# Performance work log

Measured on AMD Instinct MI355X. Metric: run time of the kernel, lower is better.

The kernel has to match this reference:

```python
import jax, jax.numpy as jnp
import numpy as np

TARGET_FRAMES = 16
VOXEL_LAMBDA = 20.0
CONF_THRESHOLD = 0.1
CONF_PERCENTILE = 50.0
G = 48  # per-axis voxel grid cap (lambda=20 => ~20-40 occupied cells/axis for randn points)


def setup_inputs() -> dict:
    key = jax.random.key(0)
    k1, k2, k3, k4, k5 = jax.random.split(key, 5)
    B, S, H, W = 1, 128, 224, 224
    return {
        "depth": jax.random.uniform(k1, (B, S, H, W, 1), dtype=jnp.float32),
        "depth_conf": jax.random.uniform(k2, (B, S, H, W), dtype=jnp.float32),
        "world_points": jax.random.normal(k3, (B, S, H, W, 3), dtype=jnp.float32),
        "world_points_conf": jax.random.uniform(k4, (B, S, H, W), dtype=jnp.float32),
        "pose_enc": jax.random.normal(k5, (B, S, 9), dtype=jnp.float32),
    }


def _voxel_occupancy(world_points, world_points_conf):
    # world_points: [1,S,H,W,3], conf: [1,S,H,W]
    pts = world_points[0].reshape(world_points.shape[1], -1, 3)   # [S, HW, 3]
    conf = world_points_conf[0].reshape(world_points.shape[1], -1)  # [S, HW]
    # per-frame confidence filter: conf > thr AND conf >= per-frame percentile
    pct = jnp.quantile(conf, CONF_PERCENTILE / 100.0, axis=1)       # [S]
    valid = (conf > CONF_THRESHOLD) & (conf >= pct[:, None])        # [S, HW]
    big = jnp.float32(1e30)
    pmin = jnp.min(jnp.where(valid[..., None], pts, big), axis=(0, 1))   # [3]
    pmax = jnp.max(jnp.where(valid[..., None], pts, -big), axis=(0, 1))  # [3]
    voxel_size = jnp.min(pmax - pmin) / VOXEL_LAMBDA  # adaptive voxel size
    idx = jnp.floor((pts - pmin) / voxel_size).astype(jnp.int32)
    idx = jnp.clip(idx, 0, G - 1)
    vid = (idx[..., 0] * G + idx[..., 1]) * G + idx[..., 2]  # [S, HW]
    V = G * G * G
    vid = jnp.where(valid, vid, V)  # invalid points -> trash bin V
    S = pts.shape[0]
    occ = jnp.zeros((S, V + 1), dtype=bool).at[jnp.arange(S)[:, None], vid].set(True)
    return occ[:, :V]  # [S, V] per-frame voxel occupancy bitmaps


def _greedy_max_coverage(occ, k):
    S, V = occ.shape

    def step(carry, _):
        covered, selected = carry  # [V] bool, [S] bool
        gains = jnp.sum(occ & ~covered[None, :], axis=1).astype(jnp.float32)  # [S]
        gains = jnp.where(selected, -1.0, gains)
        best = jnp.argmax(gains)  # first max == greedy in-order tie-break
        covered = covered | occ[best]
        selected = selected.at[best].set(True)
        return (covered, selected), (best.astype(jnp.int32), gains[best])

    (covered, _), (sel, scores) = jax.lax.scan(
        step, (jnp.zeros((V,), bool), jnp.zeros((S,), bool)), None, length=k)
    return sel, scores, covered


def reference(depth, depth_conf, world_points, world_points_conf, pose_enc):
    occ = _voxel_occupancy(world_points, world_points_conf)
    sel, scores, covered = _greedy_max_coverage(occ, TARGET_FRAMES)
    total_coverage = jnp.sum(covered).astype(jnp.int32)
    # selected_indices [1,K], coverage_scores [1,K], total_coverage scalar
    return sel[None, :], scores[None, :], total_coverage
```

## Files before the change

### kernel.cpp

```cpp
#include <hip/hip_runtime.h>
#include <cstdint>

#define S_FRAMES 128
#define HW       50176
#define NGRP     12544
#define HALFG    6272
#define NBINS    4096
#define CAP      512
#define KSEL     16
#define VBW      1568

#define PLW      1024u
#define RQ       13

#define PL_OFF   0u
#define MM_OFF   (256u*PLW)
#define UWI_OFF  (MM_OFF + 1024u)
#define PCT_OFF  (UWI_OFF + 16u)
#define VB_OFF   (PCT_OFF + 128u)
#define ZWORDS   (MM_OFF + 1024u + 16u)

__device__ __forceinline__ unsigned fkey(float f) {
    unsigned u = __float_as_uint(f);
    return (u & 0x80000000u) ? ~u : (u | 0x80000000u);
}
__device__ __forceinline__ float funkey(unsigned k) {
    unsigned u = (k & 0x80000000u) ? (k & 0x7fffffffu) : ~k;
    return __uint_as_float(u);
}

__global__ __launch_bounds__(1024) void pct_kernel(const float* __restrict__ conf,
                                                   float* __restrict__ pct,
                                                   unsigned* __restrict__ ws) {
    const int s = blockIdx.x;
    const int tid = threadIdx.x;
    const int lane = tid & 63, wid = tid >> 6;
    const float4* c4 = (const float4*)(conf + (size_t)s * HW);

    for (unsigned i = tid; i < 2057u; i += 1024u) {
        unsigned idx = (unsigned)s * 2057u + i;
        if (idx < ZWORDS) ws[idx] = 0u;
    }

    __shared__ unsigned hist[NBINS];
    __shared__ unsigned wtot[16];
    __shared__ unsigned woff[16];
    __shared__ float    list[CAP];
    __shared__ unsigned cnt;
    __shared__ int      rbin[2];
    __shared__ unsigned rcum[2];
    __shared__ float    ab[2];

    for (int b = tid; b < NBINS; b += 1024) hist[b] = 0;
    if (tid == 0) cnt = 0;
    __syncthreads();

    for (int g = tid; g < NGRP; g += 1024) {
        float4 v = c4[g];
        int b0 = min(max((int)(v.x * 4096.0f), 0), NBINS - 1);
        int b1 = min(max((int)(v.y * 4096.0f), 0), NBINS - 1);
        int b2 = min(max((int)(v.z * 4096.0f), 0), NBINS - 1);
        int b3 = min(max((int)(v.w * 4096.0f), 0), NBINS - 1);
        atomicAdd(&hist[b0], 1u); atomicAdd(&hist[b1], 1u);
        atomicAdd(&hist[b2], 1u); atomicAdd(&hist[b3], 1u);
    }
    __syncthreads();

    unsigned chunk = hist[tid * 4] + hist[tid * 4 + 1] + hist[tid * 4 + 2] + hist[tid * 4 + 3];
    unsigned x = chunk;
#pragma unroll
    for (int m = 1; m < 64; m <<= 1) {
        unsigned y = (unsigned)__shfl_up((int)x, m);
        if (lane >= m) x += y;
    }
    if (lane == 63) wtot[wid] = x;
    __syncthreads();
    if (tid < 16) {
        unsigned acc = 0;
        for (int w = 0; w < tid; w++) acc += wtot[w];
        woff[tid] = acc;
    }
    __syncthreads();
    unsigned excl = x - chunk + woff[wid];

    const unsigned R0 = 25087u, R1 = 25088u;
#pragma unroll
    for (int r = 0; r < 2; r++) {
        unsigned rr = r ? R1 : R0;
        if (rr >= excl && rr < excl + chunk) {
            unsigned cum = excl;
            for (int j = 0; j < 4; j++) {
                unsigned h = hist[tid * 4 + j];
                if (rr < cum + h) { rbin[r] = tid * 4 + j; rcum[r] = cum; break; }
                cum += h;
            }
        }
    }
    __syncthreads();

    const int blo = rbin[0], bhi = rbin[1];
    const unsigned cumLo = rcum[0];

    for (int g = tid; g < NGRP; g += 1024) {
        float4 v = c4[g];
        float vv[4] = {v.x, v.y, v.z, v.w};
#pragma unroll
        for (int j = 0; j < 4; j++) {
            int b = min(max((int)(vv[j] * 4096.0f), 0), NBINS - 1);
            if (b >= blo && b <= bhi) {
                unsigned pos = atomicAdd(&cnt, 1u);
                if (pos < CAP) list[pos] = vv[j];
            }
        }
    }
    __syncthreads();

    const int n = (int)min(cnt, (unsigned)CAP);
    const int r0 = (int)(R0 - cumLo), r1 = (int)(R1 - cumLo);
    for (int e = tid; e < n; e += 1024) {
        float xx = list[e];
        int rank = 0;
        for (int j = 0; j < n; j++) {
            float y = list[j];
            rank += (y < xx) || (y == xx && j < e);
        }
        if (rank == r0) ab[0] = xx;
        if (rank == r1) ab[1] = xx;
    }
    __syncthreads();
    if (tid == 0) pct[s] = 0.5f * ab[0] + 0.5f * ab[1];
}

__global__ __launch_bounds__(256) void minmax_kernel(const float* __restrict__ wp,
                                                     const float* __restrict__ conf,
                                                     const float* __restrict__ pct,
                                                     unsigned* __restrict__ ws) {
    const int s = blockIdx.y;
    const int tid = threadIdx.x;
    const int gidx = blockIdx.x * 256 + tid;
    const float pc = pct[s];
    const size_t base = (size_t)s * HW;

    const float4 cf = ((const float4*)(conf + base))[gidx];
    const float4* wp4 = (const float4*)(wp + base * 3) + (size_t)gidx * 3;
    const float4 a = wp4[0], b = wp4[1], d = wp4[2];

    const float BIG = 3.402823466e38f;
    float mnx = BIG, mny = BIG, mnz = BIG;
    float mxx = -BIG, mxy = -BIG, mxz = -BIG;

    float px[4] = {a.x, a.w, b.z, d.y};
    float py[4] = {a.y, b.x, b.w, d.z};
    float pz[4] = {a.z, b.y, d.x, d.w};
    float cc[4] = {cf.x, cf.y, cf.z, cf.w};
    unsigned nib = 0;
#pragma unroll
    for (int j = 0; j < 4; j++) {
        bool v = (cc[j] > 0.1f) && (cc[j] >= pc);
        nib |= (v ? 1u : 0u) << j;
        float x = v ? px[j] : BIG, y = v ? py[j] : BIG, z = v ? pz[j] : BIG;
        mnx = fminf(mnx, x); mny = fminf(mny, y); mnz = fminf(mnz, z);
        x = v ? px[j] : -BIG; y = v ? py[j] : -BIG; z = v ? pz[j] : -BIG;
        mxx = fmaxf(mxx, x); mxy = fmaxf(mxy, y); mxz = fmaxf(mxz, z);
    }

    __shared__ unsigned vbw[32];
    if (tid < 32) vbw[tid] = 0;
    __syncthreads();
    if (nib) atomicOr(&vbw[tid >> 3], nib << ((tid & 7) * 4));

#pragma unroll
    for (int m = 32; m >= 1; m >>= 1) {
        mnx = fminf(mnx, __shfl_xor(mnx, m)); mny = fminf(mny, __shfl_xor(mny, m));
        mnz = fminf(mnz, __shfl_xor(mnz, m));
        mxx = fmaxf(mxx, __shfl_xor(mxx, m)); mxy = fmaxf(mxy, __shfl_xor(mxy, m));
        mxz = fmaxf(mxz, __shfl_xor(mxz, m));
    }
    __shared__ float red[4][6];
    if ((tid & 63) == 0) {
        int w = tid >> 6;
        red[w][0] = mnx; red[w][1] = mny; red[w][2] = mnz;
        red[w][3] = mxx; red[w][4] = mxy; red[w][5] = mxz;
    }
    __syncthreads();
    if (tid < 32)
        ws[VB_OFF + (unsigned)s * 1568u + (unsigned)blockIdx.x * 32u + tid] = vbw[tid];
    if (tid == 0) {
        float r0 = red[0][0], r1 = red[0][1], r2 = red[0][2];
        float r3 = red[0][3], r4 = red[0][4], r5 = red[0][5];
        for (int w = 1; w < 4; w++) {
            r0 = fminf(r0, red[w][0]); r1 = fminf(r1, red[w][1]); r2 = fminf(r2, red[w][2]);
            r3 = fmaxf(r3, red[w][3]); r4 = fmaxf(r4, red[w][4]); r5 = fmaxf(r5, red[w][5]);
        }
        unsigned* slot = ws + MM_OFF + (unsigned)((blockIdx.x + blockIdx.y * 49) & 63) * 16;
        atomicMax(slot + 0, fkey(-r0));
        atomicMax(slot + 1, fkey(-r1));
        atomicMax(slot + 2, fkey(-r2));
        atomicMax(slot + 3, fkey(r3));
        atomicMax(slot + 4, fkey(r4));
        atomicMax(slot + 5, fkey(r5));
    }
}

__global__ __launch_bounds__(1024) void voxel_kernel(const float* __restrict__ wp,
                                                     unsigned* __restrict__ ws) {
    const int s = blockIdx.x >> 1;
    const int part = blockIdx.x & 1;
    const int tid = threadIdx.x;

    __shared__ unsigned bm[PLW];
    __shared__ float prm[4];
    __shared__ int   dsh[3];
    bm[tid] = 0;

    if (tid < 64) {
        const unsigned* sl = ws + MM_OFF + (unsigned)tid * 16;
        unsigned k0 = sl[0], k1 = sl[1], k2 = sl[2], k3 = sl[3], k4 = sl[4], k5 = sl[5];
#pragma unroll
        for (int m = 32; m >= 1; m >>= 1) {
            k0 = max(k0, (unsigned)__shfl_xor((int)k0, m));
            k1 = max(k1, (unsigned)__shfl_xor((int)k1, m));
            k2 = max(k2, (unsigned)__shfl_xor((int)k2, m));
            k3 = max(k3, (unsigned)__shfl_xor((int)k3, m));
            k4 = max(k4, (unsigned)__shfl_xor((int)k4, m));
            k5 = max(k5, (unsigned)__shfl_xor((int)k5, m));
        }
        if (tid == 0) {
            float p0 = -funkey(k0), p1 = -funkey(k1), p2 = -funkey(k2);
            float e0 = funkey(k3) - p0, e1 = funkey(k4) - p1, e2 = funkey(k5) - p2;
            float vs = fminf(e0, fminf(e1, e2)) / 20.0f;
            int Dx = min(48, (int)floorf(e0 / vs) + 1);
            int Dy = min(48, (int)floorf(e1 / vs) + 1);
            int Dz = min(48, (int)floorf(e2 / vs) + 1);
            int D  = Dx * Dy * Dz;
            prm[0] = p0; prm[1] = p1; prm[2] = p2; prm[3] = vs;
            dsh[0] = Dy; dsh[1] = Dz;
            unsigned uw = (unsigned)((D + 31) >> 5);
            dsh[2] = (int)min(uw, PLW);
            if (blockIdx.x == 0) ws[UWI_OFF] = uw;
        }
    }
    __syncthreads();

    const float pmx = prm[0], pmy = prm[1], pmz = prm[2], vs = prm[3];
    const int Dy = dsh[0], Dz = dsh[1], UWs = dsh[2];
    const size_t base = (size_t)s * HW;
    const float4* w4 = (const float4*)(wp + base * 3);
    const unsigned* vb = ws + VB_OFF + (unsigned)s * 1568u;

#pragma unroll 1
    for (int k = 0; k < 7; k++) {
        int gl = k * 1024 + tid;
        if (gl >= HALFG) break;
        int g = part * HALFG + gl;
        const float4* wg = w4 + (size_t)g * 3;
        float4 a = wg[0], b = wg[1], d = wg[2];
        unsigned nib = (vb[g >> 3] >> ((g & 7) * 4)) & 0xFu;
        if (nib) {
            float px[4] = {a.x, a.w, b.z, d.y};
            float py[4] = {a.y, b.x, b.w, d.z};
            float pz[4] = {a.z, b.y, d.x, d.w};
#pragma unroll
            for (int j = 0; j < 4; j++) {
                if ((nib >> j) & 1u) {
                    int ix = min(max((int)floorf((px[j] - pmx) / vs), 0), 47);
                    int iy = min(max((int)floorf((py[j] - pmy) / vs), 0), 47);
                    int iz = min(max((int)floorf((pz[j] - pmz) / vs), 0), 47);
                    int vid = (ix * Dy + iy) * Dz + iz;
                    if ((unsigned)vid < PLW * 32u)
                        atomicOr(&bm[vid >> 5], 1u << (vid & 31));
                }
            }
        }
    }
    __syncthreads();

    unsigned* occ = ws + PL_OFF + (unsigned)blockIdx.x * PLW;
    for (int w = tid; w < UWs; w += 1024) occ[w] = bm[w];
}

__global__ __launch_bounds__(1024, 1) void greedy1_kernel(unsigned* __restrict__ ws,
                                                          float* __restrict__ out) {
    const int tid = threadIdx.x;
    const int f = tid >> 3, sl = tid & 7;
    unsigned UW = ws[UWI_OFF];
    if (UW > PLW) UW = PLW;

    __shared__ unsigned cov[PLW];
    __shared__ int gains[S_FRAMES];
    __shared__ unsigned bestsh;

    for (int w = tid; w < (int)PLW; w += 1024) cov[w] = 0u;
    bool selF = false;
    int best = -1;

    if (UW <= 8u * RQ * 4u) {
        uint4 occw[RQ];
        const uint4* myA = (const uint4*)(ws + PL_OFF + (unsigned)(f * 2 + 0) * PLW) + sl * RQ;
        const uint4* myB = (const uint4*)(ws + PL_OFF + (unsigned)(f * 2 + 1) * PLW) + sl * RQ;
#pragma unroll
        for (int j = 0; j < RQ; j++) {
            uint4 a4 = myA[j], b4 = myB[j];
            occw[j].x = a4.x | b4.x; occw[j].y = a4.y | b4.y;
            occw[j].z = a4.z | b4.z; occw[j].w = a4.w | b4.w;
        }
        __syncthreads();

        for (int it = 0; it < KSEL; it++) {
            if (best >= 0 && f == best) {
#pragma unroll
                for (int j = 0; j < RQ; j++) {
                    int w = (sl * RQ + j) * 4;
                    cov[w] |= occw[j].x; cov[w + 1] |= occw[j].y;
                    cov[w + 2] |= occw[j].z; cov[w + 3] |= occw[j].w;
                }
            }
            __syncthreads();
            int g = 0;
#pragma unroll
            for (int j = 0; j < RQ; j++) {
                int w = (sl * RQ + j) * 4;
                g += __popc(occw[j].x & ~cov[w]) + __popc(occw[j].y & ~cov[w + 1])
                   + __popc(occw[j].z & ~cov[w + 2]) + __popc(occw[j].w & ~cov[w + 3]);
            }
            g += __shfl_xor(g, 1); g += __shfl_xor(g, 2); g += __shfl_xor(g, 4);
            if (sl == 0) gains[f] = selF ? -1 : g;
            __syncthreads();
            if (tid < 64) {
                int g1 = gains[tid], g2 = gains[tid + 64];
                unsigned k1 = (g1 < 0) ? 0u : (((unsigned)g1 << 7) | (unsigned)(127 - tid));
                unsigned k2 = (g2 < 0) ? 0u : (((unsigned)g2 << 7) | (unsigned)(63 - tid));
                unsigned k = max(k1, k2);
#pragma unroll
                for (int m = 32; m >= 1; m >>= 1) k = max(k, (unsigned)__shfl_xor((int)k, m));
                if (tid == 0) {
                    bestsh = k;
                    out[it] = (float)(127 - (int)(k & 127u));
                    out[KSEL + it] = (float)(k >> 7);
                }
            }
            __syncthreads();
            best = 127 - (int)(bestsh & 127u);
            if (f == best) selF = true;
        }
        if (f == best) {
#pragma unroll
            for (int j = 0; j < RQ; j++) {
                int w = (sl * RQ + j) * 4;
                cov[w] |= occw[j].x; cov[w + 1] |= occw[j].y;
                cov[w + 2] |= occw[j].z; cov[w + 3] |= occw[j].w;
            }
        }
        __syncthreads();
        if (f == 0) {
            int t = 0;
#pragma unroll
            for (int j = 0; j < RQ; j++) {
                int w = (sl * RQ + j) * 4;
                t += __popc(cov[w]) + __popc(cov[w + 1]) + __popc(cov[w + 2]) + __popc(cov[w + 3]);
            }
            t += __shfl_xor(t, 1); t += __shfl_xor(t, 2); t += __shfl_xor(t, 4);
            if (sl == 0) out[2 * KSEL] = (float)t;
        }
    } else {
        const int Q = (int)((UW + 31) >> 5);
        const uint4* myA = (const uint4*)(ws + PL_OFF + (unsigned)(f * 2 + 0) * PLW) + sl * Q;
        const uint4* myB = (const uint4*)(ws + PL_OFF + (unsigned)(f * 2 + 1) * PLW) + sl * Q;
        __syncthreads();

        for (int it = 0; it < KSEL; it++) {
            if (best >= 0 && f == best) {
                const uint4* bA = (const uint4*)(ws + PL_OFF + (unsigned)(best * 2 + 0) * PLW) + sl * Q;
                const uint4* bB = (const uint4*)(ws + PL_OFF + (unsigned)(best * 2 + 1) * PLW) + sl * Q;
#pragma unroll 4
                for (int j = 0; j < Q; j++) {
                    uint4 oa = bA[j], ob = bB[j];
                    int w = (sl * Q + j) * 4;
                    cov[w] |= oa.x | ob.x; cov[w + 1] |= oa.y | ob.y;
                    cov[w + 2] |= oa.z | ob.z; cov[w + 3] |= oa.w | ob.w;
                }
            }
            __syncthreads();
            int g = 0;
#pragma unroll 4
            for (int j = 0; j < Q; j++) {
                uint4 oa = myA[j], ob = myB[j];
                int w = (sl * Q + j) * 4;
                g += __popc((oa.x | ob.x) & ~cov[w]) + __popc((oa.y | ob.y) & ~cov[w + 1])
                   + __popc((oa.z | ob.z) & ~cov[w + 2]) + __popc((oa.w | ob.w) & ~cov[w + 3]);
            }
            g += __shfl_xor(g, 1); g += __shfl_xor(g, 2); g += __shfl_xor(g, 4);
            if (sl == 0) gains[f] = selF ? -1 : g;
            __syncthreads();
            if (tid < 64) {
                int g1 = gains[tid], g2 = gains[tid + 64];
                unsigned k1 = (g1 < 0) ? 0u : (((unsigned)g1 << 7) | (unsigned)(127 - tid));
                unsigned k2 = (g2 < 0) ? 0u : (((unsigned)g2 << 7) | (unsigned)(63 - tid));
                unsigned k = max(k1, k2);
#pragma unroll
                for (int m = 32; m >= 1; m >>= 1) k = max(k, (unsigned)__shfl_xor((int)k, m));
                if (tid == 0) {
                    bestsh = k;
                    out[it] = (float)(127 - (int)(k & 127u));
                    out[KSEL + it] = (float)(k >> 7);
                }
            }
            __syncthreads();
            best = 127 - (int)(bestsh & 127u);
            if (f == best) selF = true;
        }
        if (f == best) {
            const uint4* bA = (const uint4*)(ws + PL_OFF + (unsigned)(best * 2 + 0) * PLW) + sl * Q;
            const uint4* bB = (const uint4*)(ws + PL_OFF + (unsigned)(best * 2 + 1) * PLW) + sl * Q;
#pragma unroll 4
            for (int j = 0; j < Q; j++) {
                uint4 oa = bA[j], ob = bB[j];
                int w = (sl * Q + j) * 4;
                cov[w] |= oa.x | ob.x; cov[w + 1] |= oa.y | ob.y;
                cov[w + 2] |= oa.z | ob.z; cov[w + 3] |= oa.w | ob.w;
            }
        }
        __syncthreads();
        if (f == 0) {
            int t = 0;
#pragma unroll 4
            for (int j = 0; j < Q; j++) {
                int w = (sl * Q + j) * 4;
                t += __popc(cov[w]) + __popc(cov[w + 1]) + __popc(cov[w + 2]) + __popc(cov[w + 3]);
            }
            t += __shfl_xor(t, 1); t += __shfl_xor(t, 2); t += __shfl_xor(t, 4);
            if (sl == 0) out[2 * KSEL] = (float)t;
        }
    }
}

extern "C" void kernel_launch(void* const* d_in, const int* in_sizes, int n_in,
                              void* d_out, int out_size, void* d_ws, size_t ws_size,
                              hipStream_t stream) {
    const float* wp   = (const float*)d_in[2];
    const float* conf = (const float*)d_in[3];
    float* out = (float*)d_out;
    unsigned* ws = (unsigned*)d_ws;
    float* pct = (float*)(ws + PCT_OFF);

    pct_kernel<<<128, 1024, 0, stream>>>(conf, pct, ws);
    minmax_kernel<<<dim3(49, 128), 256, 0, stream>>>(wp, conf, pct, ws);
    voxel_kernel<<<256, 1024, 0, stream>>>(wp, ws);
    greedy1_kernel<<<1, 1024, 0, stream>>>(ws, out);
}
```

Measured before the change: 227.6 us.

## Split per-frame confidence histogram into quarter-frame blocks before percentile select

```diff
diff --git a/kernel.cpp b/kernel.cpp
--- a/kernel.cpp
+++ b/kernel.cpp
@@ -4,6 +4,7 @@
 #define S_FRAMES 128
 #define HW       50176
 #define NGRP     12544
+#define QGRP     3136
 #define HALFG    6272
 #define NBINS    4096
 #define CAP      512
@@ -18,6 +19,7 @@
 #define UWI_OFF  (MM_OFF + 1024u)
 #define PCT_OFF  (UWI_OFF + 16u)
 #define VB_OFF   (PCT_OFF + 128u)
+#define H4_OFF   (VB_OFF + 128u*VBW)
 #define ZWORDS   (MM_OFF + 1024u + 16u)
 
 __device__ __forceinline__ unsigned fkey(float f) {
@@ -29,18 +31,45 @@
     return __uint_as_float(u);
 }
 
-__global__ __launch_bounds__(1024) void pct_kernel(const float* __restrict__ conf,
-                                                   float* __restrict__ pct,
-                                                   unsigned* __restrict__ ws) {
+__global__ __launch_bounds__(1024) void hist4_kernel(const float* __restrict__ conf,
+                                                     unsigned* __restrict__ ws) {
+    const int s = blockIdx.x >> 2;
+    const int q = blockIdx.x & 3;
+    const int tid = threadIdx.x;
+    const float4* c4 = (const float4*)(conf + (size_t)s * HW);
+
+    if (tid < 515) {
+        unsigned idx = (unsigned)blockIdx.x * 515u + tid;
+        if (idx < ZWORDS) ws[idx] = 0u;
+    }
+
+    __shared__ unsigned hist[NBINS];
+    for (int b = tid; b < NBINS; b += 1024) hist[b] = 0;
+    __syncthreads();
+
+    const int g0 = q * QGRP;
+    for (int gl = tid; gl < QGRP; gl += 1024) {
+        float4 v = c4[g0 + gl];
+        int b0 = min(max((int)(v.x * 4096.0f), 0), NBINS - 1);
+        int b1 = min(max((int)(v.y * 4096.0f), 0), NBINS - 1);
+        int b2 = min(max((int)(v.z * 4096.0f), 0), NBINS - 1);
+        int b3 = min(max((int)(v.w * 4096.0f), 0), NBINS - 1);
+        atomicAdd(&hist[b0], 1u); atomicAdd(&hist[b1], 1u);
+        atomicAdd(&hist[b2], 1u); atomicAdd(&hist[b3], 1u);
+    }
+    __syncthreads();
+
+    unsigned* out = ws + H4_OFF + (unsigned)blockIdx.x * NBINS;
+    for (int b = tid; b < NBINS; b += 1024) out[b] = hist[b];
+}
+
+__global__ __launch_bounds__(1024) void select_kernel(const float* __restrict__ conf,
+                                                      float* __restrict__ pct,
+                                                      unsigned* __restrict__ ws) {
     const int s = blockIdx.x;
     const int tid = threadIdx.x;
     const int lane = tid & 63, wid = tid >> 6;
     const float4* c4 = (const float4*)(conf + (size_t)s * HW);
-
-    for (unsigned i = tid; i < 2057u; i += 1024u) {
-        unsigned idx = (unsigned)s * 2057u + i;
-        if (idx < ZWORDS) ws[idx] = 0u;
-    }
 
     __shared__ unsigned hist[NBINS];
     __shared__ unsigned wtot[16];
@@ -51,19 +80,13 @@
     __shared__ unsigned rcum[2];
     __shared__ float    ab[2];
 
-    for (int b = tid; b < NBINS; b += 1024) hist[b] = 0;
+    const unsigned* q0 = ws + H4_OFF + (unsigned)(s * 4 + 0) * NBINS;
+    const unsigned* q1 = ws + H4_OFF + (unsigned)(s * 4 + 1) * NBINS;
+    const unsigned* q2 = ws + H4_OFF + (unsigned)(s * 4 + 2) * NBINS;
+    const unsigned* q3 = ws + H4_OFF + (unsigned)(s * 4 + 3) * NBINS;
+    for (int b = tid; b < NBINS; b += 1024)
+        hist[b] = q0[b] + q1[b] + q2[b] + q3[b];
     if (tid == 0) cnt = 0;
-    __syncthreads();
-
-    for (int g = tid; g < NGRP; g += 1024) {
-        float4 v = c4[g];
-        int b0 = min(max((int)(v.x * 4096.0f), 0), NBINS - 1);
-        int b1 = min(max((int)(v.y * 4096.0f), 0), NBINS - 1);
-        int b2 = min(max((int)(v.z * 4096.0f), 0), NBINS - 1);
-        int b3 = min(max((int)(v.w * 4096.0f), 0), NBINS - 1);
-        atomicAdd(&hist[b0], 1u); atomicAdd(&hist[b1], 1u);
-        atomicAdd(&hist[b2], 1u); atomicAdd(&hist[b3], 1u);
-    }
     __syncthreads();
 
     unsigned chunk = hist[tid * 4] + hist[tid * 4 + 1] + hist[tid * 4 + 2] + hist[tid * 4 + 3];
@@ -443,7 +466,8 @@
     unsigned* ws = (unsigned*)d_ws;
     float* pct = (float*)(ws + PCT_OFF);
 
-    pct_kernel<<<128, 1024, 0, stream>>>(conf, pct, ws);
+    hist4_kernel<<<512, 1024, 0, stream>>>(conf, ws);
+    select_kernel<<<128, 1024, 0, stream>>>(conf, pct, ws);
     minmax_kernel<<<dim3(49, 128), 256, 0, stream>>>(wp, conf, pct, ws);
     voxel_kernel<<<256, 1024, 0, stream>>>(wp, ws);
     greedy1_kernel<<<1, 1024, 0, stream>>>(ws, out);
```

Result: no change. 230.8 us (+1.4%).
